# Kernel tuning notes

Hardware: AMD Instinct MI355X
Metric: run time of the kernel (lower is better)

The kernel has to match this reference:

```python
import jax, jax.numpy as jnp
import numpy as np

HEADS = 16
NUM_LANDMARKS = 64
PINV_ITERS = 6
D_MODEL = 1024


def _moore_penrose_pinv(x, num_iters):
    # Newton-Schulz iteration: V <- 0.25*V @ (13I - KV @ (15I - KV @ (7I - KV)))
    m = x.shape[-1]
    I = jnp.eye(m, dtype=x.dtype)
    V = x
    for _ in range(num_iters):
        KV = x @ V  # [..., m, m]
        V = 0.25 * V @ (13.0 * I - KV @ (15.0 * I - KV @ (7.0 * I - KV)))
    return V


def setup_inputs() -> dict:
    key = jax.random.key(0)
    k1, k2, k3 = jax.random.split(key, 3)
    b, n, d = 4, 4096, D_MODEL
    hidden_states = jax.random.normal(k1, (b, n, d), dtype=jnp.float32)
    Wqkv = jax.random.normal(k2, (d, 3 * d), dtype=jnp.float32) * 0.02
    bqkv = jnp.zeros((3 * d,), dtype=jnp.float32)
    Wout = jax.random.normal(k3, (d, d), dtype=jnp.float32) * 0.02
    bout = jnp.zeros((d,), dtype=jnp.float32)
    return {"hidden_states": hidden_states, "Wqkv": Wqkv, "bqkv": bqkv,
            "Wout": Wout, "bout": bout}


def reference(hidden_states, Wqkv, bqkv, Wout, bout):
    b, n, d = hidden_states.shape
    h, m = HEADS, NUM_LANDMARKS
    dh = d // h
    scale = 1.0 / np.sqrt(dh).astype(np.float32)
    # n is a multiple of m by construction, so the torch padding branch is a no-op.
    l = n // m  # tokens per landmark group

    qkv = hidden_states @ Wqkv + bqkv  # [b, n, 3d]
    q, k, v = jnp.split(qkv, 3, axis=-1)

    def to_heads(t):  # [b, n, d] -> [b, h, n, dh]
        return t.reshape(b, n, h, dh).transpose(0, 2, 1, 3)

    q, k, v = to_heads(q), to_heads(k), to_heads(v)
    q = q * scale

    # Landmarks: mean over contiguous groups of l tokens (sum / l in original).
    q_l = q.reshape(b, h, m, l, dh).mean(axis=3)  # [b, h, m, dh]
    k_l = k.reshape(b, h, m, l, dh).mean(axis=3)

    sim1 = jnp.einsum('bhid,bhjd->bhij', q, k_l)    # [b, h, n, m]
    sim2 = jnp.einsum('bhid,bhjd->bhij', q_l, k_l)  # [b, h, m, m]
    sim3 = jnp.einsum('bhid,bhjd->bhij', q_l, k)    # [b, h, m, n]

    attn1 = jax.nn.softmax(sim1, axis=-1)
    attn2 = jax.nn.softmax(sim2, axis=-1)
    attn3 = jax.nn.softmax(sim3, axis=-1)

    attn2_inv = _moore_penrose_pinv(attn2, PINV_ITERS)

    # out = attn1 @ attn2_inv @ (attn3 @ v), cheapest association
    out = attn1 @ (attn2_inv @ (attn3 @ v))  # [b, h, n, dh]
    out = out.transpose(0, 2, 1, 3).reshape(b, n, d)
    out = out @ Wout + bout
    return out
```

## Files before the change

kernel.cpp:

```cpp
#include <hip/hip_runtime.h>
#include <cstdint>

typedef unsigned short u16;
typedef __attribute__((ext_vector_type(8))) short s16x8;
typedef __attribute__((ext_vector_type(4))) float f32x4;

#define NTOK 4096
#define DH   64
#define DM   1024
#define NH   16

static __device__ __forceinline__ float b2f(u16 u){ return __uint_as_float(((unsigned)u)<<16); }
static __device__ __forceinline__ u16 f2b(float f){
  unsigned u = __float_as_uint(f);
  return (u16)((u + 0x7FFFu + ((u>>16)&1u)) >> 16);
}

static __device__ __forceinline__ void gload_lds16(const void* g, void* l) {
  __builtin_amdgcn_global_load_lds(
      (const __attribute__((address_space(1))) unsigned*)(uintptr_t)g,
      (__attribute__((address_space(3))) unsigned*)(uintptr_t)l, 16, 0, 0);
}

static __device__ __forceinline__ s16x8 ld8(const u16* p){ return *(const s16x8*)(const void*)p; }

__global__ __launch_bounds__(256) void k_pre(const float* __restrict__ hs, u16* __restrict__ Xb,
                                             float* __restrict__ Xl,
                                             const float* __restrict__ Wqkv, u16* __restrict__ WqkvT,
                                             const float* __restrict__ Wout, u16* __restrict__ WoutT) {
  __shared__ float tile[64][65];
  const int bid = blockIdx.x, t = threadIdx.x;
  if (bid < 1024) {
    const int grp = bid >> 2;
    const int d = (bid & 3)*256 + t;
    const float* p = hs + (long)grp*64*DM + d;
    u16* xo = Xb + (long)grp*64*DM + d;
    float s = 0.f;
    #pragma unroll 8
    for (int i = 0; i < 64; ++i) {
      const float v = p[(long)i*DM];
      s += v;
      xo[(long)i*DM] = f2b(v);
    }
    Xl[(long)grp*DM + d] = s * (1.0f/64.0f);
    return;
  }
  const float* in; u16* out; int R, C, tc, tr;
  if (bid < 1792) { const int x = bid - 1024; in = Wqkv; out = WqkvT; R = 1024; C = 3072; tc = x % 48; tr = x / 48; }
  else            { const int x = bid - 1792; in = Wout; out = WoutT; R = 1024; C = 1024; tc = x & 15;  tr = x >> 4; }
  const int cx = t & 63, ry = t >> 6;
  #pragma unroll
  for (int p = 0; p < 16; ++p) {
    const int row = p*4 + ry;
    tile[row][cx] = in[(long)(tr*64 + row)*C + tc*64 + cx];
  }
  __syncthreads();
  #pragma unroll
  for (int p = 0; p < 16; ++p) {
    const int orow = p*4 + ry;
    out[(long)(tc*64 + orow)*R + tr*64 + cx] = f2b(tile[cx][orow]);
  }
}

__global__ __launch_bounds__(256) void k_lproj2(const float* __restrict__ Xl, const float* __restrict__ Wqkv,
                                                float* __restrict__ psum) {
  __shared__ __align__(16) float Xs[32][68];
  const int t = threadIdx.x;
  const int wcol = blockIdx.x*256 + t;
  const int r0 = blockIdx.y*32;
  const int kbase = blockIdx.z*128;
  float acc[32];
  #pragma unroll
  for (int r = 0; r < 32; ++r) acc[r] = 0.f;
  for (int k0 = kbase; k0 < kbase + 128; k0 += 64) {
    __syncthreads();
    for (int idx = t; idx < 2048; idx += 256)
      Xs[idx>>6][idx&63] = Xl[(long)(r0 + (idx>>6))*DM + k0 + (idx&63)];
    __syncthreads();
    for (int kk = 0; kk < 64; kk += 4) {
      f32x4 wv;
      #pragma unroll
      for (int j = 0; j < 4; ++j) wv[j] = Wqkv[(long)(k0+kk+j)*3072 + wcol];
      #pragma unroll
      for (int r = 0; r < 32; ++r) {
        const f32x4 xv = *(const f32x4*)&Xs[r][kk];
        acc[r] += xv[0]*wv[0] + xv[1]*wv[1] + xv[2]*wv[2] + xv[3]*wv[3];
      }
    }
  }
  float* po = psum + ((long)blockIdx.z*256 + r0)*2048 + wcol;
  #pragma unroll
  for (int r = 0; r < 32; ++r) po[(long)r*2048] = acc[r];
}

__global__ __launch_bounds__(256) void k_lreduce(const float* __restrict__ psum, const float* __restrict__ bqkv,
                                                 float* __restrict__ qlf, float* __restrict__ klf,
                                                 u16* __restrict__ qlb, u16* __restrict__ klb) {
  const long idx = (long)blockIdx.x*256 + threadIdx.x;
  const int row = (int)(idx >> 11), col = (int)(idx & 2047);
  float s = 0.f;
  #pragma unroll
  for (int z = 0; z < 8; ++z) s += psum[((long)z*256 + row)*2048 + col];
  const int isq = (col < 1024) ? 1 : 0;
  float val = s + bqkv[col];
  if (isq) val *= 0.125f;
  const int b = row >> 6, lm = row & 63;
  const int c2 = col & 1023, h = c2 >> 6, dh = c2 & 63;
  const long o = (((long)b*NH + h)*64 + lm)*64 + dh;
  if (isq) { qlf[o] = val; qlb[o] = f2b(val); }
  else     { klf[o] = val; klb[o] = f2b(val); }
}

template<int EPI>
__global__ __launch_bounds__(512, 2) void k_gemm256(
    const u16* __restrict__ A, const u16* __restrict__ Bt, const float* __restrict__ bias,
    int N, float* __restrict__ outF, u16* __restrict__ outQ, u16* __restrict__ outK, u16* __restrict__ outV)
{
  __shared__ __align__(16) u16 lds[4*16384];
  const int K = 1024;
  const int t = threadIdx.x;
  const int lane = t & 63;
  const int wid = t >> 6;
  const int c = lane & 15, g = lane >> 4;
  const int wm = wid >> 2, wn = wid & 3;
  const int fid = blockIdx.y*64 + blockIdx.x;
  const int nbx = ((fid & 7) << 3) | ((fid >> 3) & 7);
  const int nby = fid >> 6;
  const long arow0 = (long)nbx * 256;
  const long brow0 = (long)nby * 256;
  char* ldsb = (char*)lds;

  const int srow = t >> 2;
  const int schunk = (t & 3) ^ ((srow >> 1) & 3);
  const u16* gA0 = A  + (arow0 + srow)*K       + schunk*8;
  const u16* gA1 = A  + (arow0 + 128 + srow)*K + schunk*8;
  const u16* gB0 = Bt + (brow0 + srow)*K       + schunk*8;
  const u16* gB1 = Bt + (brow0 + 128 + srow)*K + schunk*8;
  const int dstoff = t*16;

#define STAGE_A(kt) { char* bse = ldsb + ((kt)&3)*32768; \
    gload_lds16(gA0 + (kt)*32, bse + dstoff); \
    gload_lds16(gA1 + (kt)*32, bse + 8192 + dstoff); }
#define STAGE_B(kt) { char* bse = ldsb + ((kt)&3)*32768 + 16384; \
    gload_lds16(gB0 + (kt)*32, bse + dstoff); \
    gload_lds16(gB1 + (kt)*32, bse + 8192 + dstoff); }

  const int gs = g ^ ((c >> 1) & 3);
  int aoff[2][4], boff[4];
  #pragma unroll
  for (int mi = 0; mi < 4; ++mi) {
    aoff[0][mi] = (0*128 + wm*64 + mi*16 + c)*64 + gs*16;
    aoff[1][mi] = (1*128 + wm*64 + mi*16 + c)*64 + gs*16;
    boff[mi]    = 16384 + (wn*64 + mi*16 + c)*64 + gs*16;
  }

  f32x4 acc0[4][4] = {};
  f32x4 acc1[4][4] = {};

  STAGE_A(0); STAGE_B(0); STAGE_A(1); STAGE_B(1); STAGE_A(2); STAGE_B(2);
  asm volatile("s_waitcnt vmcnt(8)" ::: "memory");
  __builtin_amdgcn_s_barrier();

  s16x8 af[4], bfr[4], af2[4];
  #pragma unroll
  for (int mi = 0; mi < 4; ++mi) af[mi]  = *(const s16x8*)(ldsb + aoff[0][mi]);
  #pragma unroll
  for (int ni = 0; ni < 4; ++ni) bfr[ni] = *(const s16x8*)(ldsb + boff[ni]);

  for (int kt = 0; kt < 32; ++kt) {
    char* buf  = ldsb + (kt&3)*32768;
    char* bufn = ldsb + ((kt+1)&3)*32768;
    if (kt + 3 < 32) { STAGE_A(kt+3) STAGE_B(kt+3) }
    asm volatile("s_waitcnt lgkmcnt(0)" ::: "memory");
    __builtin_amdgcn_sched_barrier(0);
    #pragma unroll
    for (int mi = 0; mi < 4; ++mi) af2[mi] = *(const s16x8*)(buf + aoff[1][mi]);
    __builtin_amdgcn_sched_barrier(0);
    __builtin_amdgcn_s_setprio(1);
    #pragma unroll
    for (int mi = 0; mi < 4; ++mi)
      #pragma unroll
      for (int ni = 0; ni < 4; ++ni)
        acc0[mi][ni] = __builtin_amdgcn_mfma_f32_16x16x32_bf16(af[mi], bfr[ni], acc0[mi][ni], 0, 0, 0);
    __builtin_amdgcn_s_setprio(0);
    asm volatile("s_waitcnt lgkmcnt(0)" ::: "memory");
    __builtin_amdgcn_sched_barrier(0);
    if (kt <= 28)      { asm volatile("s_waitcnt vmcnt(8)" ::: "memory"); }
    else if (kt == 29) { asm volatile("s_waitcnt vmcnt(4)" ::: "memory"); }
    else if (kt == 30) { asm volatile("s_waitcnt vmcnt(0)" ::: "memory"); }
    if (kt < 31) __builtin_amdgcn_s_barrier();
    s16x8 nf[4], nb[4];
    if (kt < 31) {
      #pragma unroll
      for (int mi = 0; mi < 4; ++mi) nf[mi] = *(const s16x8*)(bufn + aoff[0][mi]);
      #pragma unroll
      for (int ni = 0; ni < 4; ++ni) nb[ni] = *(const s16x8*)(bufn + boff[ni]);
    }
    __builtin_amdgcn_sched_barrier(0);
    __builtin_amdgcn_s_setprio(1);
    #pragma unroll
    for (int mi = 0; mi < 4; ++mi)
      #pragma unroll
      for (int ni = 0; ni < 4; ++ni)
        acc1[mi][ni] = __builtin_amdgcn_mfma_f32_16x16x32_bf16(af2[mi], bfr[ni], acc1[mi][ni], 0, 0, 0);
    __builtin_amdgcn_s_setprio(0);
    if (kt < 31) {
      #pragma unroll
      for (int mi = 0; mi < 4; ++mi) { af[mi] = nf[mi]; bfr[mi] = nb[mi]; }
    }
  }
#undef STAGE_A
#undef STAGE_B

  if (EPI == 0) {
    const int tensor = (int)(brow0 >> 10);
    if (tensor == 2) {
      __syncthreads();
      u16* wlds = lds + wid*4224;
      const int hbase = (int)((brow0 + wn*64) & 1023);
      const int head = hbase >> 6;
      #pragma unroll
      for (int ph = 0; ph < 2; ++ph) {
        const long grow0 = arow0 + ph*128 + wm*64;
        const int b = (int)(grow0 >> 12), tok0r = (int)(grow0 & 4095);
        #pragma unroll
        for (int mi = 0; mi < 4; ++mi)
          #pragma unroll
          for (int ni = 0; ni < 4; ++ni) {
            const float bv = bias[brow0 + wn*64 + ni*16 + c];
            const f32x4 a = ph ? acc1[mi][ni] : acc0[mi][ni];
            #pragma unroll
            for (int r = 0; r < 4; ++r)
              wlds[(mi*16 + g*4 + r)*66 + ni*16 + c] = f2b(a[r] + bv);
          }
        asm volatile("s_waitcnt lgkmcnt(0)" ::: "memory");
        u16* vbase = outV + (((long)b*NH + head)*DH)*NTOK + tok0r;
        #pragma unroll
        for (int j = 0; j < 8; ++j) {
          const int d = j*8 + (lane >> 3);
          const int tk = (lane & 7)*8;
          s16x8 vv;
          #pragma unroll
          for (int s2 = 0; s2 < 8; ++s2) vv[s2] = (short)wlds[(tk + s2)*66 + d];
          *(s16x8*)(vbase + (long)d*NTOK + tk) = vv;
        }
        asm volatile("s_waitcnt lgkmcnt(0)" ::: "memory");
      }
    } else {
      u16* dst = (tensor == 0) ? outQ : outK;
      const float mul = (tensor == 0) ? 0.125f : 1.0f;
      #pragma unroll
      for (int ph = 0; ph < 2; ++ph)
        #pragma unroll
        for (int mi = 0; mi < 4; ++mi) {
          const int rowb = ph*128 + wm*64 + mi*16 + g*4;
          #pragma unroll
          for (int ni = 0; ni < 4; ++ni) {
            const long gcol = brow0 + wn*64 + ni*16 + c;
            const int c2 = (int)(gcol & 1023);
            const int head = c2 >> 6, dh = c2 & 63;
            const float bv = bias[gcol];
            const f32x4 a = ph ? acc1[mi][ni] : acc0[mi][ni];
            #pragma unroll
            for (int r = 0; r < 4; ++r) {
              const long grow = arow0 + rowb + r;
              const int b = (int)(grow >> 12), tok = (int)(grow & 4095);
              dst[(((long)b*NH + head)*NTOK + tok)*DH + dh] = f2b((a[r] + bv)*mul);
            }
          }
        }
    }
  } else {
    #pragma unroll
    for (int ph = 0; ph < 2; ++ph)
      #pragma unroll
      for (int mi = 0; mi < 4; ++mi) {
        const int rowb = ph*128 + wm*64 + mi*16 + g*4;
        #pragma unroll
        for (int ni = 0; ni < 4; ++ni) {
          const long gcol = brow0 + wn*64 + ni*16 + c;
          const float bv = bias[gcol];
          const f32x4 a = ph ? acc1[mi][ni] : acc0[mi][ni];
          #pragma unroll
          for (int r = 0; r < 4; ++r) {
            const long grow = arow0 + rowb + r;
            outF[grow*N + gcol] = a[r] + bv;
          }
        }
      }
  }
}

#define PST 68
static __device__ __forceinline__ void mm_nn8(const float* A, const float* B, float* C, int t) {
  const int lane = t & 63, j0 = (t >> 6) << 3;
  float acc[8];
  #pragma unroll
  for (int j = 0; j < 8; ++j) acc[j] = 0.f;
  for (int k = 0; k < 64; k += 4) {
    const f32x4 a4 = *(const f32x4*)&A[lane*PST + k];
    #pragma unroll
    for (int dk = 0; dk < 4; ++dk) {
      const float a = a4[dk];
      const float* br = &B[(k + dk)*PST + j0];
      const f32x4 b0 = *(const f32x4*)(br);
      const f32x4 b1 = *(const f32x4*)(br + 4);
      #pragma unroll
      for (int qq = 0; qq < 4; ++qq) { acc[qq] += a*b0[qq]; acc[4+qq] += a*b1[qq]; }
    }
  }
  #pragma unroll
  for (int j = 0; j < 8; ++j) C[lane*PST + j0 + j] = acc[j];
}
static __device__ __forceinline__ void mm_nt8(const float* A, const float* B, float* C, int t) {
  const int lane = t & 63, j0 = (t >> 6) << 3;
  float acc[8];
  #pragma unroll
  for (int j = 0; j < 8; ++j) acc[j] = 0.f;
  for (int k = 0; k < 64; k += 4) {
    const f32x4 a4 = *(const f32x4*)&A[lane*PST + k];
    #pragma unroll
    for (int jj = 0; jj < 8; ++jj) {
      const f32x4 b4 = *(const f32x4*)&B[(j0 + jj)*PST + k];
      acc[jj] += a4[0]*b4[0] + a4[1]*b4[1] + a4[2]*b4[2] + a4[3]*b4[3];
    }
  }
  #pragma unroll
  for (int j = 0; j < 8; ++j) C[lane*PST + j0 + j] = acc[j];
}
static __device__ __forceinline__ void mm_nn4(const float* A, const float* B, float* C, int t) {
  const int lane = t & 63, j0 = (t >> 6) << 2;
  float acc[4] = {0.f, 0.f, 0.f, 0.f};
  for (int k = 0; k < 64; k += 4) {
    const f32x4 a4 = *(const f32x4*)&A[lane*PST + k];
    #pragma unroll
    for (int dk = 0; dk < 4; ++dk) {
      const f32x4 b0 = *(const f32x4*)&B[(k + dk)*PST + j0];
      #pragma unroll
      for (int q = 0; q < 4; ++q) acc[q] += a4[dk]*b0[q];
    }
  }
  #pragma unroll
  for (int j = 0; j < 4; ++j) C[lane*PST + j0 + j] = acc[j];
}

__global__ __launch_bounds__(512) void k_pa(const float* __restrict__ qlf, const float* __restrict__ klf,
                                            float* __restrict__ a2inv,
                                            const u16* __restrict__ qlb, const u16* __restrict__ kk,
                                            const u16* __restrict__ vt,
                                            float* __restrict__ zp, float* __restrict__ sp) {
  __shared__ __align__(16) char smem[87040];
  const int t = threadIdx.x;
  if (blockIdx.x < 64) {
    float* Xb = (float*)smem;
    float* Vb = Xb + 64*PST;
    float* T1 = Vb + 64*PST;
    float* T2 = T1 + 64*PST;
    float* T3 = T2 + 64*PST;
    const int bh = blockIdx.x;
    const float* ql = qlf + (long)bh*4096;
    const float* kl = klf + (long)bh*4096;
    for (int i = t; i < 4096; i += 512) { T1[(i>>6)*PST + (i&63)] = ql[i]; T2[(i>>6)*PST + (i&63)] = kl[i]; }
    __syncthreads();
    mm_nt8(T1, T2, Xb, t);
    __syncthreads();
    if (t < 64) {
      float mx = -1e30f;
      for (int j = 0; j < 64; ++j) mx = fmaxf(mx, Xb[t*PST + j]);
      float s = 0.f;
      for (int j = 0; j < 64; ++j) { const float e = expf(Xb[t*PST + j] - mx); Xb[t*PST + j] = e; s += e; }
      const float inv = 1.0f/s;
      for (int j = 0; j < 64; ++j) Xb[t*PST + j] *= inv;
    }
    __syncthreads();
    for (int i = t; i < 4096; i += 512) { const int r = i>>6, cc = i&63; Vb[r*PST+cc] = Xb[r*PST+cc]; }
    __syncthreads();
    for (int it = 0; it < 6; ++it) {
      mm_nn8(Xb, Vb, T1, t);  __syncthreads();
      for (int i = t; i < 4096; i += 512) { const int r=i>>6, cc=i&63; T2[r*PST+cc] = (r==cc?7.0f:0.0f) - T1[r*PST+cc]; }
      __syncthreads();
      mm_nn8(T1, T2, T3, t);  __syncthreads();
      for (int i = t; i < 4096; i += 512) { const int r=i>>6, cc=i&63; T2[r*PST+cc] = (r==cc?15.0f:0.0f) - T3[r*PST+cc]; }
      __syncthreads();
      mm_nn8(T1, T2, T3, t);  __syncthreads();
      for (int i = t; i < 4096; i += 512) { const int r=i>>6, cc=i&63; T2[r*PST+cc] = (r==cc?13.0f:0.0f) - T3[r*PST+cc]; }
      __syncthreads();
      mm_nn8(Vb, T2, T3, t);  __syncthreads();
      for (int i = t; i < 4096; i += 512) { const int r=i>>6, cc=i&63; Vb[r*PST+cc] = 0.25f*T3[r*PST+cc]; }
      __syncthreads();
    }
    for (int i = t; i < 4096; i += 512) a2inv[(long)bh*4096 + i] = Vb[(i>>6)*PST + (i&63)];
    return;
  }
  float* Zlp = (float*)smem;
  float* Slp = (float*)(smem + 65536);
  char*  Plb = smem + 66560;
  const int abid = blockIdx.x - 64;
  const int bh = abid >> 3, qt = abid & 7;
  if (t < 256) {
    const int w = t >> 6, lane = t & 63;
    const int c = lane & 15, g = lane >> 4;
    s16x8 aq[4][2];
    const u16* qlp = qlb + (long)bh*4096;
    #pragma unroll
    for (int mi = 0; mi < 4; ++mi)
      #pragma unroll
      for (int ks = 0; ks < 2; ++ks)
        aq[mi][ks] = ld8(qlp + (mi*16 + c)*64 + ks*32 + g*8);

    f32x4 zacc[4][4] = {};
    float sl[4][4] = {};
    const u16* kp = kk + (long)bh*NTOK*DH;
    const u16* vp = vt + (long)bh*DH*NTOK;
    char* pbase = Plb + w*5120;
    const int tok00 = qt*512 + w*128;

    for (int it = 0; it < 4; ++it) {
      const int t0 = tok00 + it*32;
      f32x4 sacc[4][2] = {};
      s16x8 kb[2][2];
      #pragma unroll
      for (int cg = 0; cg < 2; ++cg)
        #pragma unroll
        for (int ks = 0; ks < 2; ++ks)
          kb[cg][ks] = ld8(kp + (long)(t0 + cg*16 + c)*64 + ks*32 + g*8);
      #pragma unroll
      for (int cg = 0; cg < 2; ++cg)
        #pragma unroll
        for (int ks = 0; ks < 2; ++ks)
          #pragma unroll
          for (int mi = 0; mi < 4; ++mi)
            sacc[mi][cg] = __builtin_amdgcn_mfma_f32_16x16x32_bf16(aq[mi][ks], kb[cg][ks], sacc[mi][cg], 0, 0, 0);
      #pragma unroll
      for (int mi = 0; mi < 4; ++mi)
        #pragma unroll
        for (int r = 0; r < 4; ++r) {
          const int row = mi*16 + g*4 + r;
          const float p0 = __expf(sacc[mi][0][r]);
          const float p1 = __expf(sacc[mi][1][r]);
          sl[mi][r] += p0 + p1;
          char* base = pbase + row*80;
          *(u16*)(base + c*2)      = f2b(p0);
          *(u16*)(base + 32 + c*2) = f2b(p1);
        }
      s16x8 pa[4];
      #pragma unroll
      for (int mi = 0; mi < 4; ++mi) pa[mi] = *(const s16x8*)(pbase + (mi*16 + c)*80 + g*16);
      #pragma unroll
      for (int ni = 0; ni < 4; ++ni) {
        const s16x8 vb = ld8(vp + (long)(ni*16 + c)*NTOK + t0 + g*8);
        #pragma unroll
        for (int mi = 0; mi < 4; ++mi)
          zacc[mi][ni] = __builtin_amdgcn_mfma_f32_16x16x32_bf16(pa[mi], vb, zacc[mi][ni], 0, 0, 0);
      }
    }
    #pragma unroll
    for (int mi = 0; mi < 4; ++mi)
      #pragma unroll
      for (int r = 0; r < 4; ++r) {
        float s = sl[mi][r];
        s += __shfl_xor(s, 1); s += __shfl_xor(s, 2); s += __shfl_xor(s, 4); s += __shfl_xor(s, 8);
        sl[mi][r] = s;
      }
    #pragma unroll
    for (int mi = 0; mi < 4; ++mi)
      #pragma unroll
      for (int ni = 0; ni < 4; ++ni)
        #pragma unroll
        for (int r = 0; r < 4; ++r)
          Zlp[w*4096 + (mi*16 + g*4 + r)*64 + ni*16 + c] = zacc[mi][ni][r];
    if (c == 0)
      #pragma unroll
      for (int mi = 0; mi < 4; ++mi)
        #pragma unroll
        for (int r = 0; r < 4; ++r)
          Slp[w*64 + mi*16 + g*4 + r] = sl[mi][r];
  }
  __syncthreads();
  float* zpp = zp + (long)abid*4096;
  for (int i = t; i < 4096; i += 512)
    zpp[i] = Zlp[i] + Zlp[4096 + i] + Zlp[8192 + i] + Zlp[12288 + i];
  if (t < 64) sp[(long)abid*64 + t] = Slp[t] + Slp[64 + t] + Slp[128 + t] + Slp[192 + t];
}

__global__ __launch_bounds__(1024) void k_w2(const float* __restrict__ a2inv,
                                             const float* __restrict__ zp, const float* __restrict__ sp,
                                             u16* __restrict__ w2t) {
  __shared__ __align__(16) float Ai[64*PST];
  __shared__ __align__(16) float Zi[64*PST];
  __shared__ __align__(16) float Ci[64*PST];
  __shared__ float Ss[64];
  const int bh = blockIdx.x, t = threadIdx.x;
  if (t < 64) {
    float ss = 0.f;
    #pragma unroll
    for (int qt = 0; qt < 8; ++qt) ss += sp[(long)(bh*8 + qt)*64 + t];
    Ss[t] = 1.0f / ss;
  }
  for (int i = t; i < 4096; i += 1024)
    Ai[(i>>6)*PST + (i&63)] = a2inv[(long)bh*4096 + i];
  __syncthreads();
  for (int i = t; i < 4096; i += 1024) {
    float zs = 0.f;
    #pragma unroll
    for (int qt = 0; qt < 8; ++qt) zs += zp[((long)(bh*8 + qt))*4096 + i];
    Zi[(i>>6)*PST + (i&63)] = zs * Ss[i>>6];
  }
  __syncthreads();
  mm_nn4(Ai, Zi, Ci, t);
  __syncthreads();
  for (int i = t; i < 4096; i += 1024) { const int r = i>>6, cc = i&63; w2t[(long)bh*4096 + cc*64 + r] = f2b(Ci[r*PST + cc]); }
}

#define P1ST 144
__global__ __launch_bounds__(256) void k_attn1(const u16* __restrict__ q, const u16* __restrict__ klb,
                                               const u16* __restrict__ w2t, u16* __restrict__ ao) {
  __shared__ __align__(16) u16 Pl[4][64][72];
  const int bx = blockIdx.x, bh = bx >> 4, tt = bx & 15;
  const int b = bh >> 4, h = bh & 15;
  const int t = threadIdx.x, w = t >> 6, lane = t & 63;
  const int c = lane & 15, g = lane >> 4;
  const int tok0 = tt*256 + w*64;
  const u16* qp  = q + ((long)bh*NTOK + tok0)*DH;
  const u16* klp = klb + (long)bh*4096;
  const u16* wp  = w2t + (long)bh*4096;
  char* pbase = (char*)&Pl[w][0][0];

  s16x8 aq[4][2], kb[4][2], wb[4][2];
  #pragma unroll
  for (int i = 0; i < 4; ++i)
    #pragma unroll
    for (int ks = 0; ks < 2; ++ks) {
      aq[i][ks] = ld8(qp + (long)(i*16 + c)*DH + ks*32 + g*8);
      kb[i][ks] = ld8(klp + (i*16 + c)*64 + ks*32 + g*8);
      wb[i][ks] = ld8(wp  + (i*16 + c)*64 + ks*32 + g*8);
    }
  f32x4 sacc[4][4] = {};
  #pragma unroll
  for (int ks = 0; ks < 2; ++ks)
    #pragma unroll
    for (int mi = 0; mi < 4; ++mi)
      #pragma unroll
      for (int ni = 0; ni < 4; ++ni)
        sacc[mi][ni] = __builtin_amdgcn_mfma_f32_16x16x32_bf16(aq[mi][ks], kb[ni][ks], sacc[mi][ni], 0, 0, 0);

  float rs[4][4];
  #pragma unroll
  for (int mi = 0; mi < 4; ++mi)
    #pragma unroll
    for (int r = 0; r < 4; ++r) {
      const int row = mi*16 + g*4 + r;
      char* base = pbase + row*P1ST;
      float ssum = 0.f;
      #pragma unroll
      for (int ni = 0; ni < 4; ++ni) {
        const float p = __expf(sacc[mi][ni][r]);
        ssum += p;
        *(u16*)(base + (ni*16 + c)*2) = f2b(p);
      }
      ssum += __shfl_xor(ssum, 1); ssum += __shfl_xor(ssum, 2);
      ssum += __shfl_xor(ssum, 4); ssum += __shfl_xor(ssum, 8);
      rs[mi][r] = ssum;
    }
  __builtin_amdgcn_s_barrier();
  s16x8 pa[4][2];
  #pragma unroll
  for (int mi = 0; mi < 4; ++mi)
    #pragma unroll
    for (int ks = 0; ks < 2; ++ks)
      pa[mi][ks] = *(const s16x8*)(pbase + (mi*16 + c)*P1ST + ks*64 + g*16);
  f32x4 oacc[4][4] = {};
  #pragma unroll
  for (int ks = 0; ks < 2; ++ks)
    #pragma unroll
    for (int mi = 0; mi < 4; ++mi)
      #pragma unroll
      for (int ni = 0; ni < 4; ++ni)
        oacc[mi][ni] = __builtin_amdgcn_mfma_f32_16x16x32_bf16(pa[mi][ks], wb[ni][ks], oacc[mi][ni], 0, 0, 0);

  u16* op = ao + (long)b*NTOK*DM + (long)h*64;
  #pragma unroll
  for (int mi = 0; mi < 4; ++mi)
    #pragma unroll
    for (int r = 0; r < 4; ++r) {
      const int tok = tok0 + mi*16 + g*4 + r;
      const float inv = 1.0f / rs[mi][r];
      #pragma unroll
      for (int ni = 0; ni < 4; ++ni)
        op[(long)tok*DM + ni*16 + c] = f2b(oacc[mi][ni][r] * inv);
    }
}

extern "C" void kernel_launch(void* const* d_in, const int* in_sizes, int n_in,
                              void* d_out, int out_size, void* d_ws, size_t ws_size,
                              hipStream_t stream) {
  const float* hs   = (const float*)d_in[0];
  const float* Wqkv = (const float*)d_in[1];
  const float* bqkv = (const float*)d_in[2];
  const float* Wout = (const float*)d_in[3];
  const float* bout = (const float*)d_in[4];
  float* out = (float*)d_out;
  char* w = (char*)d_ws;

  u16*  Xb    = (u16*)(w);
  float* zp   = (float*)(w);
  float* sp   = (float*)(w + 8388608L);
  u16*  WqkvT = (u16*)(w + 33554432L);
  u16*  WoutT = (u16*)(w + 39845888L);
  u16*  q     = (u16*)(w + 41943040L);
  float* psum = (float*)(w + 41943040L);
  u16*  k     = (u16*)(w + 75497472L);
  float* Xl   = (float*)(w + 109051904L);
  u16*  vt    = (u16*)(w + 142606336L);
  float* qlf  = (float*)(w + 176160768L);
  float* klf  = (float*)(w + 177209344L);
  u16*  qlb   = (u16*)(w + 178257920L);
  u16*  klb   = (u16*)(w + 178782208L);
  float* a2i  = (float*)(w + 179306496L);
  u16*  w2t   = (u16*)(w + 181403648L);
  u16*  ao    = (u16*)(w + 181927936L);

  k_pre<<<2048, 256, 0, stream>>>(hs, Xb, Xl, Wqkv, WqkvT, Wout, WoutT);
  k_lproj2<<<dim3(8,8,8), 256, 0, stream>>>(Xl, Wqkv, psum);
  k_lreduce<<<2048, 256, 0, stream>>>(psum, bqkv, qlf, klf, qlb, klb);
  k_gemm256<0><<<dim3(64,12), 512, 0, stream>>>(Xb, WqkvT, bqkv, 3072, nullptr, q, k, vt);
  k_pa<<<576, 512, 0, stream>>>(qlf, klf, a2i, qlb, k, vt, zp, sp);
  k_w2<<<64, 1024, 0, stream>>>(a2i, zp, sp, w2t);
  k_attn1<<<1024, 256, 0, stream>>>(q, klb, w2t, ao);
  k_gemm256<1><<<dim3(64,4), 512, 0, stream>>>(ao, WoutT, bout, 1024, out, nullptr, nullptr, nullptr);
}
```

Baseline: 334.6 us.

## Restructure 256x256 GEMM mainloop to double-buffered BK=64 with interleaved staging

Replaces the 4-stage BK=32 ring buffer of the QKV/out projection GEMM with a 2-stage BK=64 double buffer (64 KB per stage). Global-to-LDS loads for the next tile are split into four quarter-stages issued between the MFMA phases, with barriers around each. The LDS layout changes to 128-byte rows with an XOR swizzle over eight 16-byte chunks. The aim is fewer loop iterations and barriers per unit of K, and better overlap of loads with MFMAs. In exchange the prefetch depth is shallower and more s_barriers are issued per iteration, which risks exposing load latency.

```diff
diff --git a/kernel.cpp b/kernel.cpp
--- a/kernel.cpp
+++ b/kernel.cpp
@@ -116,8 +116,7 @@
     const u16* __restrict__ A, const u16* __restrict__ Bt, const float* __restrict__ bias,
     int N, float* __restrict__ outF, u16* __restrict__ outQ, u16* __restrict__ outK, u16* __restrict__ outV)
 {
-  __shared__ __align__(16) u16 lds[4*16384];
-  const int K = 1024;
+  __shared__ __align__(16) u16 lds[2*32768];
   const int t = threadIdx.x;
   const int lane = t & 63;
   const int wid = t >> 6;
@@ -130,87 +129,107 @@
   const long brow0 = (long)nby * 256;
   char* ldsb = (char*)lds;
 
-  const int srow = t >> 2;
-  const int schunk = (t & 3) ^ ((srow >> 1) & 3);
-  const u16* gA0 = A  + (arow0 + srow)*K       + schunk*8;
-  const u16* gA1 = A  + (arow0 + 128 + srow)*K + schunk*8;
-  const u16* gB0 = Bt + (brow0 + srow)*K       + schunk*8;
-  const u16* gB1 = Bt + (brow0 + 128 + srow)*K + schunk*8;
-  const int dstoff = t*16;
-
-#define STAGE_A(kt) { char* bse = ldsb + ((kt)&3)*32768; \
-    gload_lds16(gA0 + (kt)*32, bse + dstoff); \
-    gload_lds16(gA1 + (kt)*32, bse + 8192 + dstoff); }
-#define STAGE_B(kt) { char* bse = ldsb + ((kt)&3)*32768 + 16384; \
-    gload_lds16(gB0 + (kt)*32, bse + dstoff); \
-    gload_lds16(gB1 + (kt)*32, bse + 8192 + dstoff); }
-
-  const int gs = g ^ ((c >> 1) & 3);
-  int aoff[2][4], boff[4];
+  const int srow3 = t >> 3;
+  const int sch = ((t & 7) ^ (srow3 & 7)) * 8;
+  const u16* sA = A  + (arow0 + srow3)*1024 + sch;
+  const u16* sB = Bt + (brow0 + srow3)*1024 + sch;
+  const int dbase = t*16;
+
+#define STG(gp, R0, Toff, kbe, nb) { \
+    char* d0 = ldsb + (nb)*65536 + (Toff) + (R0)*128 + dbase; \
+    gload_lds16((gp) + (long)(R0)*1024 + (kbe), d0); \
+    gload_lds16((gp) + (long)((R0)+64)*1024 + (kbe), d0 + 8192); }
+
+  const int cp0 = ((g     ) ^ (c & 7)) * 16;
+  const int cp1 = ((4 | g ) ^ (c & 7)) * 16;
+  int rowA[4], rowB[4];
   #pragma unroll
   for (int mi = 0; mi < 4; ++mi) {
-    aoff[0][mi] = (0*128 + wm*64 + mi*16 + c)*64 + gs*16;
-    aoff[1][mi] = (1*128 + wm*64 + mi*16 + c)*64 + gs*16;
-    boff[mi]    = 16384 + (wn*64 + mi*16 + c)*64 + gs*16;
+    rowA[mi] = (wm*64 + mi*16 + c)*128;
+    rowB[mi] = 32768 + (wn*64 + mi*16 + c)*128;
   }
 
   f32x4 acc0[4][4] = {};
   f32x4 acc1[4][4] = {};
 
-  STAGE_A(0); STAGE_B(0); STAGE_A(1); STAGE_B(1); STAGE_A(2); STAGE_B(2);
-  asm volatile("s_waitcnt vmcnt(8)" ::: "memory");
+  STG(sB, 0, 32768, 0, 0)
+  STG(sB, 128, 32768, 0, 0)
+  STG(sA, 0, 0, 0, 0)
+  STG(sA, 128, 0, 0, 0)
+  asm volatile("s_waitcnt vmcnt(2)" ::: "memory");
   __builtin_amdgcn_s_barrier();
 
-  s16x8 af[4], bfr[4], af2[4];
-  #pragma unroll
-  for (int mi = 0; mi < 4; ++mi) af[mi]  = *(const s16x8*)(ldsb + aoff[0][mi]);
-  #pragma unroll
-  for (int ni = 0; ni < 4; ++ni) bfr[ni] = *(const s16x8*)(ldsb + boff[ni]);
-
-  for (int kt = 0; kt < 32; ++kt) {
-    char* buf  = ldsb + (kt&3)*32768;
-    char* bufn = ldsb + ((kt+1)&3)*32768;
-    if (kt + 3 < 32) { STAGE_A(kt+3) STAGE_B(kt+3) }
+  for (int it = 0; it < 16; ++it) {
+    char* buf = ldsb + (it&1)*65536;
+    const int nb = (it+1)&1;
+    const int kb1 = (it+1)*64;
+    const bool last = (it == 15);
+    s16x8 fa[4], fb[4], ga[4];
+    #pragma unroll
+    for (int mi = 0; mi < 4; ++mi) fa[mi] = *(const s16x8*)(buf + rowA[mi] + cp0);
+    #pragma unroll
+    for (int ni = 0; ni < 4; ++ni) fb[ni] = *(const s16x8*)(buf + rowB[ni] + cp0);
+    if (!last) STG(sB, 0, 32768, kb1, nb)
+    __builtin_amdgcn_s_barrier();
     asm volatile("s_waitcnt lgkmcnt(0)" ::: "memory");
     __builtin_amdgcn_sched_barrier(0);
-    #pragma unroll
-    for (int mi = 0; mi < 4; ++mi) af2[mi] = *(const s16x8*)(buf + aoff[1][mi]);
+    __builtin_amdgcn_s_setprio(1);
+    #pragma unroll
+    for (int mi = 0; mi < 4; ++mi)
+      #pragma unroll
+      for (int ni = 0; ni < 4; ++ni)
+        acc0[mi][ni] = __builtin_amdgcn_mfma_f32_16x16x32_bf16(fa[mi], fb[ni], acc0[mi][ni], 0, 0, 0);
+    __builtin_amdgcn_s_setprio(0);
+    if (last) { asm volatile("s_waitcnt vmcnt(0)" ::: "memory"); }
+    else      { asm volatile("s_waitcnt vmcnt(2)" ::: "memory"); }
+    __builtin_amdgcn_s_barrier();
+    #pragma unroll
+    for (int mi = 0; mi < 4; ++mi) ga[mi] = *(const s16x8*)(buf + rowA[mi] + 16384 + cp0);
+    if (!last) STG(sB, 128, 32768, kb1, nb)
+    __builtin_amdgcn_s_barrier();
+    asm volatile("s_waitcnt lgkmcnt(0)" ::: "memory");
     __builtin_amdgcn_sched_barrier(0);
     __builtin_amdgcn_s_setprio(1);
     #pragma unroll
     for (int mi = 0; mi < 4; ++mi)
       #pragma unroll
       for (int ni = 0; ni < 4; ++ni)
-        acc0[mi][ni] = __builtin_amdgcn_mfma_f32_16x16x32_bf16(af[mi], bfr[ni], acc0[mi][ni], 0, 0, 0);
+        acc1[mi][ni] = __builtin_amdgcn_mfma_f32_16x16x32_bf16(ga[mi], fb[ni], acc1[mi][ni], 0, 0, 0);
     __builtin_amdgcn_s_setprio(0);
+    __builtin_amdgcn_s_barrier();
+    #pragma unroll
+    for (int mi = 0; mi < 4; ++mi) fa[mi] = *(const s16x8*)(buf + rowA[mi] + cp1);
+    #pragma unroll
+    for (int ni = 0; ni < 4; ++ni) fb[ni] = *(const s16x8*)(buf + rowB[ni] + cp1);
+    if (!last) STG(sA, 0, 0, kb1, nb)
+    __builtin_amdgcn_s_barrier();
     asm volatile("s_waitcnt lgkmcnt(0)" ::: "memory");
     __builtin_amdgcn_sched_barrier(0);
-    if (kt <= 28)      { asm volatile("s_waitcnt vmcnt(8)" ::: "memory"); }
-    else if (kt == 29) { asm volatile("s_waitcnt vmcnt(4)" ::: "memory"); }
-    else if (kt == 30) { asm volatile("s_waitcnt vmcnt(0)" ::: "memory"); }
-    if (kt < 31) __builtin_amdgcn_s_barrier();
-    s16x8 nf[4], nb[4];
-    if (kt < 31) {
-      #pragma unroll
-      for (int mi = 0; mi < 4; ++mi) nf[mi] = *(const s16x8*)(bufn + aoff[0][mi]);
-      #pragma unroll
-      for (int ni = 0; ni < 4; ++ni) nb[ni] = *(const s16x8*)(bufn + boff[ni]);
-    }
+    __builtin_amdgcn_s_setprio(1);
+    #pragma unroll
+    for (int mi = 0; mi < 4; ++mi)
+      #pragma unroll
+      for (int ni = 0; ni < 4; ++ni)
+        acc0[mi][ni] = __builtin_amdgcn_mfma_f32_16x16x32_bf16(fa[mi], fb[ni], acc0[mi][ni], 0, 0, 0);
+    __builtin_amdgcn_s_setprio(0);
+    __builtin_amdgcn_s_barrier();
+    #pragma unroll
+    for (int mi = 0; mi < 4; ++mi) ga[mi] = *(const s16x8*)(buf + rowA[mi] + 16384 + cp1);
+    if (!last) STG(sA, 128, 0, kb1, nb)
+    __builtin_amdgcn_s_barrier();
+    asm volatile("s_waitcnt lgkmcnt(0)" ::: "memory");
     __builtin_amdgcn_sched_barrier(0);
     __builtin_amdgcn_s_setprio(1);
     #pragma unroll
     for (int mi = 0; mi < 4; ++mi)
       #pragma unroll
       for (int ni = 0; ni < 4; ++ni)
-        acc1[mi][ni] = __builtin_amdgcn_mfma_f32_16x16x32_bf16(af2[mi], bfr[ni], acc1[mi][ni], 0, 0, 0);
+        acc1[mi][ni] = __builtin_amdgcn_mfma_f32_16x16x32_bf16(ga[mi], fb[ni], acc1[mi][ni], 0, 0, 0);
     __builtin_amdgcn_s_setprio(0);
-    if (kt < 31) {
-      #pragma unroll
-      for (int mi = 0; mi < 4; ++mi) { af[mi] = nf[mi]; bfr[mi] = nb[mi]; }
-    }
-  }
-#undef STAGE_A
-#undef STAGE_B
+    if (!last) { asm volatile("s_waitcnt vmcnt(2)" ::: "memory"); }
+    __builtin_amdgcn_s_barrier();
+  }
+#undef STG
 
   if (EPI == 0) {
     const int tensor = (int)(brow0 >> 10);
```

Measured after the change: 324.9 us. 1.03x faster.
